# Kernel optimization log

Hardware: AMD Instinct MI355X
Metric: run time of the kernel (lower is better)

Reference implementation:

```python
import jax, jax.numpy as jnp
import numpy as np

D_MODEL = 2048
N_HEADS = 32
N_KV = 8
N_REP = N_HEADS // N_KV  # 4
HEAD_DIM = D_MODEL // N_HEADS  # 64
ROPE_BASE = 10000.0
B, T = 2, 2048


def rope_tables(seq_len, head_dim):
    inv_freq = 1.0 / (ROPE_BASE ** (jnp.arange(0, head_dim, 2, dtype=jnp.float32) / head_dim))
    t = jnp.arange(seq_len, dtype=jnp.float32)
    freqs = jnp.outer(t, inv_freq)            # [T, hd/2]
    emb = jnp.concatenate([freqs, freqs], -1)  # [T, hd]
    return jnp.cos(emb), jnp.sin(emb)


def rotate_half(x):
    x1, x2 = jnp.split(x, 2, axis=-1)
    return jnp.concatenate([-x2, x1], axis=-1)


def setup_inputs() -> dict:
    key = jax.random.key(0)
    ks = jax.random.split(key, 5)
    s = D_MODEL ** -0.5
    return {
        "x": jax.random.normal(ks[0], (B, T, D_MODEL), jnp.float32),
        "Wq": jax.random.normal(ks[1], (D_MODEL, D_MODEL), jnp.float32) * s,
        "Wk": jax.random.normal(ks[2], (D_MODEL, N_KV * HEAD_DIM), jnp.float32) * s,
        "Wv": jax.random.normal(ks[3], (D_MODEL, N_KV * HEAD_DIM), jnp.float32) * s,
        "Wo": jax.random.normal(ks[4], (D_MODEL, D_MODEL), jnp.float32) * s,
    }


def reference(x, Wq, Wk, Wv, Wo):
    Bx, Tx, C = x.shape
    # QKV projections -> [B, H, T, hd]
    q = (x @ Wq).reshape(Bx, Tx, N_HEADS, HEAD_DIM).transpose(0, 2, 1, 3)
    k = (x @ Wk).reshape(Bx, Tx, N_KV, HEAD_DIM).transpose(0, 2, 1, 3)
    v = (x @ Wv).reshape(Bx, Tx, N_KV, HEAD_DIM).transpose(0, 2, 1, 3)
    # RoPE (offset=0, no cache -> prefill path)
    cos, sin = rope_tables(Tx, HEAD_DIM)  # [T, hd]
    cos = cos[None, None]
    sin = sin[None, None]
    q = q * cos + rotate_half(q) * sin
    k = k * cos + rotate_half(k) * sin
    # Grouped causal attention without materializing expanded KV:
    # q grouped as [B, n_kv, n_rep, T, hd] shares each kv head across n_rep q heads.
    scale = HEAD_DIM ** -0.5
    qg = q.reshape(Bx, N_KV, N_REP, Tx, HEAD_DIM)
    scores = jnp.einsum('bgrtd,bgsd->bgrts', qg, k) * scale  # [B, g, r, T, S]
    causal = jnp.tril(jnp.ones((Tx, Tx), dtype=bool))
    scores = jnp.where(causal, scores, jnp.float32(-jnp.inf))
    attn = jax.nn.softmax(scores, axis=-1)
    out = jnp.einsum('bgrts,bgsd->bgrtd', attn, v)  # [B, g, r, T, hd]
    out = out.reshape(Bx, N_HEADS, Tx, HEAD_DIM).transpose(0, 2, 1, 3).reshape(Bx, Tx, C)
    return out @ Wo, k, v
```

## Files before the change

kernel.cpp:

```cpp
#include <hip/hip_runtime.h>
#include <hip/hip_bf16.h>
#include <cstdint>

typedef uint16_t u16;
typedef __attribute__((ext_vector_type(8))) __bf16 bf16x8;
typedef __attribute__((ext_vector_type(4))) float f32x4;
typedef __attribute__((ext_vector_type(16))) float f32x16;
typedef __attribute__((ext_vector_type(8))) unsigned short u16x8;

#define GLD_LDS(SRC, DST) \
  __builtin_amdgcn_global_load_lds((const __attribute__((address_space(1))) void*)(SRC), \
                                   (__attribute__((address_space(3))) void*)(DST), 16, 0, 0)

__device__ __forceinline__ u16 f2bf(float f) {
  uint32_t u = __float_as_uint(f);
  u += 0x7fffu + ((u >> 16) & 1u);
  return (u16)(u >> 16);
}

__device__ __forceinline__ uint32_t pk2(float a, float b) {
  union { __bf16 h[2]; uint32_t u; } x;
  x.h[0] = (__bf16)a; x.h[1] = (__bf16)b;
  return x.u;
}

__device__ __forceinline__ float fexp2(float x) {
#if __has_builtin(__builtin_amdgcn_exp2f)
  return __builtin_amdgcn_exp2f(x);
#else
  return exp2f(x);
#endif
}

__global__ void cast_f32_bf16(const float* __restrict__ in, u16* __restrict__ out, int n4) {
  int i = blockIdx.x * blockDim.x + threadIdx.x;
  if (i < n4) {
    const float4 v = reinterpret_cast<const float4*>(in)[i];
    ushort4 o;
    o.x = f2bf(v.x); o.y = f2bf(v.y); o.z = f2bf(v.z); o.w = f2bf(v.w);
    reinterpret_cast<ushort4*>(out)[i] = o;
  }
}

__global__ void transpose_cast(const float* __restrict__ W, u16* __restrict__ Wt, int K, int N) {
  __shared__ float tile[32][33];
  int n0 = blockIdx.x * 32, k0 = blockIdx.y * 32;
  int tx = threadIdx.x, ty = threadIdx.y;
  #pragma unroll
  for (int i = ty; i < 32; i += 8)
    tile[i][tx] = W[(size_t)(k0 + i) * N + n0 + tx];
  __syncthreads();
  #pragma unroll
  for (int i = ty; i < 32; i += 8)
    Wt[(size_t)(n0 + i) * K + k0 + tx] = f2bf(tile[tx][i]);
}

__global__ void rope_tables_k(float* __restrict__ cosT, float* __restrict__ sinT) {
  int t = blockIdx.x, i = threadIdx.x;
  float invf = powf(10000.0f, -(float)i * (1.0f / 32.0f));
  float ang = (float)t * invf;
  cosT[t * 32 + i] = cosf(ang);
  sinT[t * 32 + i] = sinf(ang);
}

__global__ __launch_bounds__(512, 2) void gemm256(const u16* __restrict__ A,
    const u16* __restrict__ Bt, float* __restrict__ C, int M, int N, int K) {
  __shared__ alignas(16) u16 Asm[2][2][256][32];
  __shared__ alignas(16) u16 Bsm[2][2][256][32];

  const int tid = threadIdx.x;
  const int l = tid & 63;
  const int w = tid >> 6;
  const int wm = w >> 2, wn = w & 3;
  const int l15 = l & 15, l4 = l >> 4;
  const int m0 = blockIdx.y * 256, n0 = blockIdx.x * 256;
  const int NT = K >> 6;

  f32x4 acc[8][4] = {};

  const int srow = tid >> 2;
  const int sg   = (tid & 3) ^ ((srow >> 1) & 3);
  const u16* Ag = A + (size_t)(m0 + srow) * K + sg * 8;
  const u16* Bg = Bt + (size_t)(n0 + srow) * K + sg * 8;
  const size_t rsk = (size_t)128 * K;
  char* AsD = (char*)&Asm[0][0][0][0] + tid * 16;
  char* BsD = (char*)&Bsm[0][0][0][0] + tid * 16;

#define STAGE_A(BUF, KH, KT) do { \
    GLD_LDS(Ag + (KT) + (KH) * 32,       AsD + ((BUF) * 2 + (KH)) * 16384); \
    GLD_LDS(Ag + (KT) + (KH) * 32 + rsk, AsD + ((BUF) * 2 + (KH)) * 16384 + 8192); \
  } while (0)
#define STAGE_B(BUF, KH, KT) do { \
    GLD_LDS(Bg + (KT) + (KH) * 32,       BsD + ((BUF) * 2 + (KH)) * 16384); \
    GLD_LDS(Bg + (KT) + (KH) * 32 + rsk, BsD + ((BUF) * 2 + (KH)) * 16384 + 8192); \
  } while (0)

  STAGE_A(0, 0, 0);  STAGE_B(0, 0, 0);
  STAGE_A(0, 1, 0);  STAGE_B(0, 1, 0);
  STAGE_A(1, 0, 64); STAGE_B(1, 0, 64);

  const int swz = (l15 >> 1) & 3;

  for (int t = 0; t < NT; ++t) {
    const int c = t & 1;
    const int ktn  = (t + 1) << 6;
    const int ktn2 = (t + 2) << 6;
    bf16x8 bfv[4], af[4];

    if (t < NT - 1) { asm volatile("s_waitcnt vmcnt(8)" ::: "memory"); }
    else            { asm volatile("s_waitcnt vmcnt(4)" ::: "memory"); }
    asm volatile("s_barrier" ::: "memory");
    #pragma unroll
    for (int mf = 0; mf < 4; ++mf)
      af[mf] = *(const bf16x8*)&Asm[c][0][wm * 128 + mf * 16 + l15][(l4 ^ swz) * 8];
    #pragma unroll
    for (int nf = 0; nf < 4; ++nf)
      bfv[nf] = *(const bf16x8*)&Bsm[c][0][wn * 64 + nf * 16 + l15][(l4 ^ swz) * 8];
    if (t + 1 < NT) STAGE_A(c ^ 1, 1, ktn);
    __builtin_amdgcn_s_setprio(1);
    #pragma unroll
    for (int mf = 0; mf < 4; ++mf)
      #pragma unroll
      for (int nf = 0; nf < 4; ++nf)
        acc[mf][nf] = __builtin_amdgcn_mfma_f32_16x16x32_bf16(af[mf], bfv[nf], acc[mf][nf], 0, 0, 0);
    __builtin_amdgcn_s_setprio(0);
    asm volatile("s_barrier" ::: "memory");

    #pragma unroll
    for (int mf = 0; mf < 4; ++mf)
      af[mf] = *(const bf16x8*)&Asm[c][0][wm * 128 + 64 + mf * 16 + l15][(l4 ^ swz) * 8];
    if (t + 1 < NT) STAGE_B(c ^ 1, 1, ktn);
    __builtin_amdgcn_s_setprio(1);
    #pragma unroll
    for (int mf = 0; mf < 4; ++mf)
      #pragma unroll
      for (int nf = 0; nf < 4; ++nf)
        acc[4 + mf][nf] = __builtin_amdgcn_mfma_f32_16x16x32_bf16(af[mf], bfv[nf], acc[4 + mf][nf], 0, 0, 0);
    __builtin_amdgcn_s_setprio(0);
    asm volatile("s_barrier" ::: "memory");

    if (t < NT - 1) { asm volatile("s_waitcnt vmcnt(8)" ::: "memory"); }
    else            { asm volatile("s_waitcnt vmcnt(0)" ::: "memory"); }
    asm volatile("s_barrier" ::: "memory");
    #pragma unroll
    for (int mf = 0; mf < 4; ++mf)
      af[mf] = *(const bf16x8*)&Asm[c][1][wm * 128 + mf * 16 + l15][(l4 ^ swz) * 8];
    #pragma unroll
    for (int nf = 0; nf < 4; ++nf)
      bfv[nf] = *(const bf16x8*)&Bsm[c][1][wn * 64 + nf * 16 + l15][(l4 ^ swz) * 8];
    if (t + 2 < NT) STAGE_A(c, 0, ktn2);
    __builtin_amdgcn_s_setprio(1);
    #pragma unroll
    for (int mf = 0; mf < 4; ++mf)
      #pragma unroll
      for (int nf = 0; nf < 4; ++nf)
        acc[mf][nf] = __builtin_amdgcn_mfma_f32_16x16x32_bf16(af[mf], bfv[nf], acc[mf][nf], 0, 0, 0);
    __builtin_amdgcn_s_setprio(0);
    asm volatile("s_barrier" ::: "memory");

    #pragma unroll
    for (int mf = 0; mf < 4; ++mf)
      af[mf] = *(const bf16x8*)&Asm[c][1][wm * 128 + 64 + mf * 16 + l15][(l4 ^ swz) * 8];
    if (t + 2 < NT) STAGE_B(c, 0, ktn2);
    __builtin_amdgcn_s_setprio(1);
    #pragma unroll
    for (int mf = 0; mf < 4; ++mf)
      #pragma unroll
      for (int nf = 0; nf < 4; ++nf)
        acc[4 + mf][nf] = __builtin_amdgcn_mfma_f32_16x16x32_bf16(af[mf], bfv[nf], acc[4 + mf][nf], 0, 0, 0);
    __builtin_amdgcn_s_setprio(0);
    asm volatile("s_barrier" ::: "memory");
  }
#undef STAGE_A
#undef STAGE_B

  #pragma unroll
  for (int mi = 0; mi < 8; ++mi)
    #pragma unroll
    for (int nf = 0; nf < 4; ++nf)
      #pragma unroll
      for (int r = 0; r < 4; ++r) {
        int row = m0 + wm * 128 + mi * 16 + l4 * 4 + r;
        int col = n0 + wn * 64 + nf * 16 + l15;
        C[(size_t)row * N + col] = acc[mi][nf][r];
      }
}

__global__ __launch_bounds__(256) void rope_scatter(const float* __restrict__ QKV,
    const float* __restrict__ cosT, const float* __restrict__ sinT,
    u16* __restrict__ Qr, u16* __restrict__ Kr,
    float* __restrict__ outK, float* __restrict__ outV) {
  const float QSCALE = 0.125f * 1.44269504088896f;
  int row = blockIdx.x;
  int b = row >> 11, t = row & 2047;
  const float* src = QKV + (size_t)row * 3072;
  int tid = threadIdx.x;
  #pragma unroll
  for (int p = tid; p < 1024; p += 256) {
    int h = p >> 5, d = p & 31;
    float c = cosT[t * 32 + d], s = sinT[t * 32 + d];
    float q0 = src[h * 64 + d], q1 = src[h * 64 + d + 32];
    size_t base = ((size_t)(b * 32 + h) * 2048 + t) * 64 + d;
    Qr[base]      = f2bf((q0 * c - q1 * s) * QSCALE);
    Qr[base + 32] = f2bf((q1 * c + q0 * s) * QSCALE);
  }
  {
    int p = tid;
    int gk = p >> 5, d = p & 31;
    float c = cosT[t * 32 + d], s = sinT[t * 32 + d];
    float k0 = src[2048 + gk * 64 + d], k1 = src[2048 + gk * 64 + d + 32];
    float r0 = k0 * c - k1 * s, r1 = k1 * c + k0 * s;
    size_t base = ((size_t)(b * 8 + gk) * 2048 + t) * 64 + d;
    Kr[base] = f2bf(r0); Kr[base + 32] = f2bf(r1);
    outK[base] = r0; outK[base + 32] = r1;
  }
  #pragma unroll
  for (int p = tid; p < 512; p += 256) {
    int gv = p >> 6, d = p & 63;
    size_t base = ((size_t)(b * 8 + gv) * 2048 + t) * 64 + d;
    outV[base] = src[2560 + gv * 64 + d];
  }
}

__global__ __launch_bounds__(256) void v_transpose(const float* __restrict__ src, u16* __restrict__ dst) {
  __shared__ float tile[64][65];
  int tt = blockIdx.x, bg = blockIdx.y;
  int tid = threadIdx.x;
  const float* sp = src + (size_t)bg * 2048 * 64 + (size_t)tt * 64 * 64;
  int tl = tid >> 2, c0 = (tid & 3) * 16;
  #pragma unroll
  for (int i = 0; i < 4; ++i) {
    float4 v = *reinterpret_cast<const float4*>(sp + (size_t)tl * 64 + c0 + i * 4);
    tile[tl][c0 + i * 4 + 0] = v.x;
    tile[tl][c0 + i * 4 + 1] = v.y;
    tile[tl][c0 + i * 4 + 2] = v.z;
    tile[tl][c0 + i * 4 + 3] = v.w;
  }
  __syncthreads();
  int d = tid >> 2, j0 = (tid & 3) * 16;
  u16x8 a, c;
  #pragma unroll
  for (int j = 0; j < 8; ++j) a[j] = f2bf(tile[j0 + j][d]);
  #pragma unroll
  for (int j = 0; j < 8; ++j) c[j] = f2bf(tile[j0 + 8 + j][d]);
  u16* dp = dst + (size_t)bg * 64 * 2048 + (size_t)d * 2048 + tt * 64 + j0;
  *reinterpret_cast<u16x8*>(dp) = a;
  *reinterpret_cast<u16x8*>(dp + 8) = c;
}

__global__ __launch_bounds__(256) void attn_kernel(
    const u16* __restrict__ Qr, const u16* __restrict__ Kr,
    const u16* __restrict__ Vt, u16* __restrict__ Ao) {
  __shared__ alignas(16) u16 Ks[2][64][72];
  __shared__ alignas(16) u16 Vs[2][64][72];

  const float FIXEDM = 24.0f;

  int bid = blockIdx.x;
  int pairI = bid >> 5;
  int sub = (bid >> 4) & 1;
  int g   = (bid >> 1) & 7;
  int b   = bid & 1;
  int tid = threadIdx.x;
  int w = tid >> 6, l = tid & 63;
  int l31 = l & 31, hi = l >> 5;
  int h = g * 4 + w;

  const u16* Kh = Kr + (size_t)(b * 8 + g) * 2048 * 64;
  const u16* Vh = Vt + (size_t)(b * 8 + g) * 64 * 2048;

  union { u16x8 u; bf16x8 v; } ones;
  #pragma unroll
  for (int i = 0; i < 8; ++i) ones.u[i] = 0x3F80;

  int srow = tid >> 2, sc0 = (tid & 3) * 16;
  const u16* Kp = Kh + (size_t)srow * 64 + sc0;
  const u16* Vp = Vh + (size_t)srow * 2048 + sc0;

  for (int half = 0; half < 2; ++half) {
    const int qc  = half ? pairI : (31 - pairI);
    const int q0w = qc * 64 + sub * 32;
    const int qg  = q0w + l31;

    const u16* Qh = Qr + ((size_t)(b * 32 + h) * 2048 + q0w) * 64;
    bf16x8 qf[4];
    #pragma unroll
    for (int t = 0; t < 4; ++t)
      qf[t] = *reinterpret_cast<const bf16x8*>(Qh + (size_t)l31 * 64 + t * 16 + hi * 8);

    f32x16 o0 = {}, o1 = {}, lacc = {};

    if (half) __syncthreads();

    {
      bf16x8 k0v = *reinterpret_cast<const bf16x8*>(Kp);
      bf16x8 k1v = *reinterpret_cast<const bf16x8*>(Kp + 8);
      bf16x8 v0v = *reinterpret_cast<const bf16x8*>(Vp);
      bf16x8 v1v = *reinterpret_cast<const bf16x8*>(Vp + 8);
      *reinterpret_cast<bf16x8*>(&Ks[0][srow][sc0]) = k0v;
      *reinterpret_cast<bf16x8*>(&Ks[0][srow][sc0 + 8]) = k1v;
      *reinterpret_cast<bf16x8*>(&Vs[0][srow][sc0]) = v0v;
      *reinterpret_cast<bf16x8*>(&Vs[0][srow][sc0 + 8]) = v1v;
    }
    __syncthreads();

    for (int s = 0; s <= qc; ++s) {
      int cur = s & 1;
      bf16x8 knx0, knx1, vnx0, vnx1;
      if (s < qc) {
        knx0 = *reinterpret_cast<const bf16x8*>(Kp + (size_t)(s + 1) * 4096);
        knx1 = *reinterpret_cast<const bf16x8*>(Kp + (size_t)(s + 1) * 4096 + 8);
        vnx0 = *reinterpret_cast<const bf16x8*>(Vp + (size_t)(s + 1) * 64);
        vnx1 = *reinterpret_cast<const bf16x8*>(Vp + (size_t)(s + 1) * 64 + 8);
      }
      int nh = (s == qc && sub == 0) ? 1 : 2;

      f32x16 s0 = {}, s1 = {};
      __builtin_amdgcn_s_setprio(1);
      #pragma unroll
      for (int t = 0; t < 4; ++t) {
        bf16x8 kf0 = *reinterpret_cast<const bf16x8*>(&Ks[cur][l31][t * 16 + hi * 8]);
        s0 = __builtin_amdgcn_mfma_f32_32x32x16_bf16(kf0, qf[t], s0, 0, 0, 0);
      }
      if (nh == 2) {
        #pragma unroll
        for (int t = 0; t < 4; ++t) {
          bf16x8 kf1 = *reinterpret_cast<const bf16x8*>(&Ks[cur][32 + l31][t * 16 + hi * 8]);
          s1 = __builtin_amdgcn_mfma_f32_32x32x16_bf16(kf1, qf[t], s1, 0, 0, 0);
        }
      }
      __builtin_amdgcn_s_setprio(0);

      if (s == qc) {
        #pragma unroll
        for (int r = 0; r < 16; ++r) {
          int kvg = s * 64 + (r & 3) + (r >> 2) * 8 + hi * 4;
          if (kvg > qg) s0[r] = -INFINITY;
        }
        if (nh == 2) {
          #pragma unroll
          for (int r = 0; r < 16; ++r) {
            int kvg = s * 64 + 32 + (r & 3) + (r >> 2) * 8 + hi * 4;
            if (kvg > qg) s1[r] = -INFINITY;
          }
        }
      }

      float p0[16], p1[16];
      #pragma unroll
      for (int r = 0; r < 16; ++r) p0[r] = fexp2(s0[r] - FIXEDM);
      if (nh == 2) {
        #pragma unroll
        for (int r = 0; r < 16; ++r) p1[r] = fexp2(s1[r] - FIXEDM);
      }

      uint32_t pkA[8], pkB[8];
      #pragma unroll
      for (int gi = 0; gi < 8; ++gi) {
        if (gi < nh * 4) {
          const float* pp = (gi < 4) ? p0 : p1;
          int base = (gi & 3) * 4;
          pkA[gi] = pk2(pp[base + 0], pp[base + 1]);
          pkB[gi] = pk2(pp[base + 2], pp[base + 3]);
        }
      }
      __builtin_amdgcn_s_setprio(1);
      #pragma unroll
      for (int kc = 0; kc < 4; ++kc) {
        if (kc < nh * 2) {
          uint32_t zA = pkA[kc * 2 + (hi ^ 1)];
          uint32_t zB = pkB[kc * 2 + (hi ^ 1)];
          uint32_t sA = (uint32_t)__shfl_xor((int)zA, 32);
          uint32_t sB = (uint32_t)__shfl_xor((int)zB, 32);
          uint32_t oA = pkA[kc * 2 + hi];
          uint32_t oB = pkB[kc * 2 + hi];
          union { uint32_t wd[4]; bf16x8 v; } pb;
          pb.wd[0] = hi ? sA : oA;
          pb.wd[1] = hi ? sB : oB;
          pb.wd[2] = hi ? oA : sA;
          pb.wd[3] = hi ? oB : sB;
          bf16x8 va0 = *reinterpret_cast<const bf16x8*>(&Vs[cur][l31][kc * 16 + hi * 8]);
          bf16x8 va1 = *reinterpret_cast<const bf16x8*>(&Vs[cur][32 + l31][kc * 16 + hi * 8]);
          o0 = __builtin_amdgcn_mfma_f32_32x32x16_bf16(va0, pb.v, o0, 0, 0, 0);
          o1 = __builtin_amdgcn_mfma_f32_32x32x16_bf16(va1, pb.v, o1, 0, 0, 0);
          lacc = __builtin_amdgcn_mfma_f32_32x32x16_bf16(ones.v, pb.v, lacc, 0, 0, 0);
        }
      }
      __builtin_amdgcn_s_setprio(0);

      if (s < qc) {
        *reinterpret_cast<bf16x8*>(&Ks[cur ^ 1][srow][sc0]) = knx0;
        *reinterpret_cast<bf16x8*>(&Ks[cur ^ 1][srow][sc0 + 8]) = knx1;
        *reinterpret_cast<bf16x8*>(&Vs[cur ^ 1][srow][sc0]) = vnx0;
        *reinterpret_cast<bf16x8*>(&Vs[cur ^ 1][srow][sc0 + 8]) = vnx1;
        __syncthreads();
      }
    }

    float inv = 1.0f / lacc[0];
    int token = b * 2048 + q0w + l31;
    u16* dst = Ao + (size_t)token * 2048 + h * 64;
    #pragma unroll
    for (int hf = 0; hf < 2; ++hf) {
      f32x16 ov = hf ? o1 : o0;
      #pragma unroll
      for (int r = 0; r < 16; r += 2) {
        int d = (r & 3) + (r >> 2) * 8 + hi * 4 + hf * 32;
        *reinterpret_cast<uint32_t*>(dst + d) = pk2(ov[r] * inv, ov[r + 1] * inv);
      }
    }
  }
}

extern "C" void kernel_launch(void* const* d_in, const int* in_sizes, int n_in,
                              void* d_out, int out_size, void* d_ws, size_t ws_size,
                              hipStream_t stream) {
  const float* x  = (const float*)d_in[0];
  const float* Wq = (const float*)d_in[1];
  const float* Wk = (const float*)d_in[2];
  const float* Wv = (const float*)d_in[3];
  const float* Wo = (const float*)d_in[4];
  float* out = (float*)d_out;

  char* ws = (char*)d_ws;
  u16*   Xb    = (u16*)(ws + 0);
  u16*   Wcat  = (u16*)(ws + 16777216);
  u16*   WoT   = (u16*)(ws + 29360128);
  float* QKV   = (float*)(ws + 37748736);
  u16*   AttnB = (u16*)(ws + 37748736);
  u16*   Qr    = (u16*)(ws + 88080384);
  u16*   Kr    = (u16*)(ws + 104857600);
  u16*   Vtr   = (u16*)(ws + 109051904);
  float* cosT  = (float*)(ws + 113246208);
  float* sinT  = (float*)(ws + 113508352);

  float* outK = out + 8388608;
  float* outV = out + 10485760;

  cast_f32_bf16<<<8192, 256, 0, stream>>>(x, Xb, 2097152);
  transpose_cast<<<dim3(64, 64), dim3(32, 8), 0, stream>>>(Wq, Wcat, 2048, 2048);
  transpose_cast<<<dim3(16, 64), dim3(32, 8), 0, stream>>>(Wk, Wcat + 2048 * 2048, 2048, 512);
  transpose_cast<<<dim3(16, 64), dim3(32, 8), 0, stream>>>(Wv, Wcat + 2560 * 2048, 2048, 512);
  transpose_cast<<<dim3(64, 64), dim3(32, 8), 0, stream>>>(Wo, WoT, 2048, 2048);
  rope_tables_k<<<2048, 32, 0, stream>>>(cosT, sinT);
  gemm256<<<dim3(12, 16), 512, 0, stream>>>(Xb, Wcat, QKV, 4096, 3072, 2048);
  rope_scatter<<<4096, 256, 0, stream>>>(QKV, cosT, sinT, Qr, Kr, outK, outV);
  v_transpose<<<dim3(32, 16), 256, 0, stream>>>(outV, Vtr);
  attn_kernel<<<512, 256, 0, stream>>>(Qr, Kr, Vtr, AttnB);
  gemm256<<<dim3(8, 16), 512, 0, stream>>>(AttnB, WoT, out, 4096, 2048, 2048);
}
```

Baseline: 238.2 us.

## Load K/V MFMA fragments directly from global memory instead of LDS staging

Removes the double-buffered LDS tiles for K and V and the per-iteration __syncthreads. Each wave now reads its MFMA operand fragments straight from global memory (relying on L1/L2 since the four waves share the same KV head). It also raises launch bounds to request 4 blocks per CU. This trades LDS traffic and barriers for redundant global loads with no software prefetch, so load latency is exposed inside the MFMA loop.

```diff
diff --git a/kernel.cpp b/kernel.cpp
--- a/kernel.cpp
+++ b/kernel.cpp
@@ -248,12 +248,9 @@
   *reinterpret_cast<u16x8*>(dp + 8) = c;
 }
 
-__global__ __launch_bounds__(256) void attn_kernel(
+__global__ __launch_bounds__(256, 4) void attn_kernel(
     const u16* __restrict__ Qr, const u16* __restrict__ Kr,
     const u16* __restrict__ Vt, u16* __restrict__ Ao) {
-  __shared__ alignas(16) u16 Ks[2][64][72];
-  __shared__ alignas(16) u16 Vs[2][64][72];
-
   const float FIXEDM = 24.0f;
 
   int bid = blockIdx.x;
@@ -269,13 +266,12 @@
   const u16* Kh = Kr + (size_t)(b * 8 + g) * 2048 * 64;
   const u16* Vh = Vt + (size_t)(b * 8 + g) * 64 * 2048;
 
+  const u16* Kl = Kh + (size_t)l31 * 64 + hi * 8;
+  const u16* Vl = Vh + (size_t)l31 * 2048 + hi * 8;
+
   union { u16x8 u; bf16x8 v; } ones;
   #pragma unroll
   for (int i = 0; i < 8; ++i) ones.u[i] = 0x3F80;
-
-  int srow = tid >> 2, sc0 = (tid & 3) * 16;
-  const u16* Kp = Kh + (size_t)srow * 64 + sc0;
-  const u16* Vp = Vh + (size_t)srow * 2048 + sc0;
 
   for (int half = 0; half < 2; ++half) {
     const int qc  = half ? pairI : (31 - pairI);
@@ -290,42 +286,22 @@
 
     f32x16 o0 = {}, o1 = {}, lacc = {};
 
-    if (half) __syncthreads();
-
-    {
-      bf16x8 k0v = *reinterpret_cast<const bf16x8*>(Kp);
-      bf16x8 k1v = *reinterpret_cast<const bf16x8*>(Kp + 8);
-      bf16x8 v0v = *reinterpret_cast<const bf16x8*>(Vp);
-      bf16x8 v1v = *reinterpret_cast<const bf16x8*>(Vp + 8);
-      *reinterpret_cast<bf16x8*>(&Ks[0][srow][sc0]) = k0v;
-      *reinterpret_cast<bf16x8*>(&Ks[0][srow][sc0 + 8]) = k1v;
-      *reinterpret_cast<bf16x8*>(&Vs[0][srow][sc0]) = v0v;
-      *reinterpret_cast<bf16x8*>(&Vs[0][srow][sc0 + 8]) = v1v;
-    }
-    __syncthreads();
-
     for (int s = 0; s <= qc; ++s) {
-      int cur = s & 1;
-      bf16x8 knx0, knx1, vnx0, vnx1;
-      if (s < qc) {
-        knx0 = *reinterpret_cast<const bf16x8*>(Kp + (size_t)(s + 1) * 4096);
-        knx1 = *reinterpret_cast<const bf16x8*>(Kp + (size_t)(s + 1) * 4096 + 8);
-        vnx0 = *reinterpret_cast<const bf16x8*>(Vp + (size_t)(s + 1) * 64);
-        vnx1 = *reinterpret_cast<const bf16x8*>(Vp + (size_t)(s + 1) * 64 + 8);
-      }
+      const u16* Ksp = Kl + (size_t)s * 4096;
+      const u16* Vsp = Vl + s * 64;
       int nh = (s == qc && sub == 0) ? 1 : 2;
 
       f32x16 s0 = {}, s1 = {};
       __builtin_amdgcn_s_setprio(1);
       #pragma unroll
       for (int t = 0; t < 4; ++t) {
-        bf16x8 kf0 = *reinterpret_cast<const bf16x8*>(&Ks[cur][l31][t * 16 + hi * 8]);
+        bf16x8 kf0 = *reinterpret_cast<const bf16x8*>(Ksp + t * 16);
         s0 = __builtin_amdgcn_mfma_f32_32x32x16_bf16(kf0, qf[t], s0, 0, 0, 0);
       }
       if (nh == 2) {
         #pragma unroll
         for (int t = 0; t < 4; ++t) {
-          bf16x8 kf1 = *reinterpret_cast<const bf16x8*>(&Ks[cur][32 + l31][t * 16 + hi * 8]);
+          bf16x8 kf1 = *reinterpret_cast<const bf16x8*>(Ksp + 2048 + t * 16);
           s1 = __builtin_amdgcn_mfma_f32_32x32x16_bf16(kf1, qf[t], s1, 0, 0, 0);
         }
       }
@@ -379,22 +355,14 @@
           pb.wd[1] = hi ? sB : oB;
           pb.wd[2] = hi ? oA : sA;
           pb.wd[3] = hi ? oB : sB;
-          bf16x8 va0 = *reinterpret_cast<const bf16x8*>(&Vs[cur][l31][kc * 16 + hi * 8]);
-          bf16x8 va1 = *reinterpret_cast<const bf16x8*>(&Vs[cur][32 + l31][kc * 16 + hi * 8]);
+          bf16x8 va0 = *reinterpret_cast<const bf16x8*>(Vsp + kc * 16);
+          bf16x8 va1 = *reinterpret_cast<const bf16x8*>(Vsp + 65536 + kc * 16);
           o0 = __builtin_amdgcn_mfma_f32_32x32x16_bf16(va0, pb.v, o0, 0, 0, 0);
           o1 = __builtin_amdgcn_mfma_f32_32x32x16_bf16(va1, pb.v, o1, 0, 0, 0);
           lacc = __builtin_amdgcn_mfma_f32_32x32x16_bf16(ones.v, pb.v, lacc, 0, 0, 0);
         }
       }
       __builtin_amdgcn_s_setprio(0);
-
-      if (s < qc) {
-        *reinterpret_cast<bf16x8*>(&Ks[cur ^ 1][srow][sc0]) = knx0;
-        *reinterpret_cast<bf16x8*>(&Ks[cur ^ 1][srow][sc0 + 8]) = knx1;
-        *reinterpret_cast<bf16x8*>(&Vs[cur ^ 1][srow][sc0]) = vnx0;
-        *reinterpret_cast<bf16x8*>(&Vs[cur ^ 1][srow][sc0 + 8]) = vnx1;
-        __syncthreads();
-      }
     }
 
     float inv = 1.0f / lacc[0];
```

Measured after the change: 388.1 us. 1.63x slower.

## Emit bf16 QKV from projection GEMM and merge attention sub-blocks into 512-thread blocks

Applied to the files above, without the earlier changes.

The QKV projection GEMM now writes bf16 instead of fp32, which halves the intermediate write and the read in rope_scatter. The returned K and V outputs are then rebuilt from bf16-rounded values, so they lose precision. Separately, the attention kernel merges the two 32-row query sub-blocks into one 512-thread block. Each K/V tile is then loaded to shared memory once for both halves, with each thread loading half as much, and the block count is halved.

```diff
diff --git a/kernel.cpp b/kernel.cpp
--- a/kernel.cpp
+++ b/kernel.cpp
@@ -16,6 +16,10 @@
   uint32_t u = __float_as_uint(f);
   u += 0x7fffu + ((u >> 16) & 1u);
   return (u16)(u >> 16);
+}
+
+__device__ __forceinline__ float bf2f(u16 u) {
+  return __uint_as_float(((uint32_t)u) << 16);
 }
 
 __device__ __forceinline__ uint32_t pk2(float a, float b) {
@@ -63,8 +67,9 @@
   sinT[t * 32 + i] = sinf(ang);
 }
 
+template<bool BF16OUT>
 __global__ __launch_bounds__(512, 2) void gemm256(const u16* __restrict__ A,
-    const u16* __restrict__ Bt, float* __restrict__ C, int M, int N, int K) {
+    const u16* __restrict__ Bt, void* __restrict__ Cv, int M, int N, int K) {
   __shared__ alignas(16) u16 Asm[2][2][256][32];
   __shared__ alignas(16) u16 Bsm[2][2][256][32];
 
@@ -182,24 +187,25 @@
       for (int r = 0; r < 4; ++r) {
         int row = m0 + wm * 128 + mi * 16 + l4 * 4 + r;
         int col = n0 + wn * 64 + nf * 16 + l15;
-        C[(size_t)row * N + col] = acc[mi][nf][r];
-      }
-}
-
-__global__ __launch_bounds__(256) void rope_scatter(const float* __restrict__ QKV,
+        if (BF16OUT) ((u16*)Cv)[(size_t)row * N + col] = f2bf(acc[mi][nf][r]);
+        else         ((float*)Cv)[(size_t)row * N + col] = acc[mi][nf][r];
+      }
+}
+
+__global__ __launch_bounds__(256) void rope_scatter(const u16* __restrict__ QKV,
     const float* __restrict__ cosT, const float* __restrict__ sinT,
     u16* __restrict__ Qr, u16* __restrict__ Kr,
     float* __restrict__ outK, float* __restrict__ outV) {
   const float QSCALE = 0.125f * 1.44269504088896f;
   int row = blockIdx.x;
   int b = row >> 11, t = row & 2047;
-  const float* src = QKV + (size_t)row * 3072;
+  const u16* src = QKV + (size_t)row * 3072;
   int tid = threadIdx.x;
   #pragma unroll
   for (int p = tid; p < 1024; p += 256) {
     int h = p >> 5, d = p & 31;
     float c = cosT[t * 32 + d], s = sinT[t * 32 + d];
-    float q0 = src[h * 64 + d], q1 = src[h * 64 + d + 32];
+    float q0 = bf2f(src[h * 64 + d]), q1 = bf2f(src[h * 64 + d + 32]);
     size_t base = ((size_t)(b * 32 + h) * 2048 + t) * 64 + d;
     Qr[base]      = f2bf((q0 * c - q1 * s) * QSCALE);
     Qr[base + 32] = f2bf((q1 * c + q0 * s) * QSCALE);
@@ -208,7 +214,7 @@
     int p = tid;
     int gk = p >> 5, d = p & 31;
     float c = cosT[t * 32 + d], s = sinT[t * 32 + d];
-    float k0 = src[2048 + gk * 64 + d], k1 = src[2048 + gk * 64 + d + 32];
+    float k0 = bf2f(src[2048 + gk * 64 + d]), k1 = bf2f(src[2048 + gk * 64 + d + 32]);
     float r0 = k0 * c - k1 * s, r1 = k1 * c + k0 * s;
     size_t base = ((size_t)(b * 8 + gk) * 2048 + t) * 64 + d;
     Kr[base] = f2bf(r0); Kr[base + 32] = f2bf(r1);
@@ -218,7 +224,7 @@
   for (int p = tid; p < 512; p += 256) {
     int gv = p >> 6, d = p & 63;
     size_t base = ((size_t)(b * 8 + gv) * 2048 + t) * 64 + d;
-    outV[base] = src[2560 + gv * 64 + d];
+    outV[base] = bf2f(src[2560 + gv * 64 + d]);
   }
 }
 
@@ -248,7 +254,7 @@
   *reinterpret_cast<u16x8*>(dp + 8) = c;
 }
 
-__global__ __launch_bounds__(256) void attn_kernel(
+__global__ __launch_bounds__(512) void attn_kernel(
     const u16* __restrict__ Qr, const u16* __restrict__ Kr,
     const u16* __restrict__ Vt, u16* __restrict__ Ao) {
   __shared__ alignas(16) u16 Ks[2][64][72];
@@ -257,14 +263,14 @@
   const float FIXEDM = 24.0f;
 
   int bid = blockIdx.x;
-  int pairI = bid >> 5;
-  int sub = (bid >> 4) & 1;
+  int pairI = bid >> 4;
   int g   = (bid >> 1) & 7;
   int b   = bid & 1;
   int tid = threadIdx.x;
   int w = tid >> 6, l = tid & 63;
   int l31 = l & 31, hi = l >> 5;
-  int h = g * 4 + w;
+  int h = g * 4 + (w & 3);
+  int sub = w >> 2;
 
   const u16* Kh = Kr + (size_t)(b * 8 + g) * 2048 * 64;
   const u16* Vh = Vt + (size_t)(b * 8 + g) * 64 * 2048;
@@ -273,7 +279,7 @@
   #pragma unroll
   for (int i = 0; i < 8; ++i) ones.u[i] = 0x3F80;
 
-  int srow = tid >> 2, sc0 = (tid & 3) * 16;
+  int srow = tid >> 3, sc0 = (tid & 7) * 8;
   const u16* Kp = Kh + (size_t)srow * 64 + sc0;
   const u16* Vp = Vh + (size_t)srow * 2048 + sc0;
 
@@ -294,24 +300,18 @@
 
     {
       bf16x8 k0v = *reinterpret_cast<const bf16x8*>(Kp);
-      bf16x8 k1v = *reinterpret_cast<const bf16x8*>(Kp + 8);
       bf16x8 v0v = *reinterpret_cast<const bf16x8*>(Vp);
-      bf16x8 v1v = *reinterpret_cast<const bf16x8*>(Vp + 8);
       *reinterpret_cast<bf16x8*>(&Ks[0][srow][sc0]) = k0v;
-      *reinterpret_cast<bf16x8*>(&Ks[0][srow][sc0 + 8]) = k1v;
       *reinterpret_cast<bf16x8*>(&Vs[0][srow][sc0]) = v0v;
-      *reinterpret_cast<bf16x8*>(&Vs[0][srow][sc0 + 8]) = v1v;
     }
     __syncthreads();
 
     for (int s = 0; s <= qc; ++s) {
       int cur = s & 1;
-      bf16x8 knx0, knx1, vnx0, vnx1;
+      bf16x8 knx, vnx;
       if (s < qc) {
-        knx0 = *reinterpret_cast<const bf16x8*>(Kp + (size_t)(s + 1) * 4096);
-        knx1 = *reinterpret_cast<const bf16x8*>(Kp + (size_t)(s + 1) * 4096 + 8);
-        vnx0 = *reinterpret_cast<const bf16x8*>(Vp + (size_t)(s + 1) * 64);
-        vnx1 = *reinterpret_cast<const bf16x8*>(Vp + (size_t)(s + 1) * 64 + 8);
+        knx = *reinterpret_cast<const bf16x8*>(Kp + (size_t)(s + 1) * 4096);
+        vnx = *reinterpret_cast<const bf16x8*>(Vp + (size_t)(s + 1) * 64);
       }
       int nh = (s == qc && sub == 0) ? 1 : 2;
 
@@ -389,10 +389,8 @@
       __builtin_amdgcn_s_setprio(0);
 
       if (s < qc) {
-        *reinterpret_cast<bf16x8*>(&Ks[cur ^ 1][srow][sc0]) = knx0;
-        *reinterpret_cast<bf16x8*>(&Ks[cur ^ 1][srow][sc0 + 8]) = knx1;
-        *reinterpret_cast<bf16x8*>(&Vs[cur ^ 1][srow][sc0]) = vnx0;
-        *reinterpret_cast<bf16x8*>(&Vs[cur ^ 1][srow][sc0 + 8]) = vnx1;
+        *reinterpret_cast<bf16x8*>(&Ks[cur ^ 1][srow][sc0]) = knx;
+        *reinterpret_cast<bf16x8*>(&Vs[cur ^ 1][srow][sc0]) = vnx;
         __syncthreads();
       }
     }
@@ -426,7 +424,7 @@
   u16*   Xb    = (u16*)(ws + 0);
   u16*   Wcat  = (u16*)(ws + 16777216);
   u16*   WoT   = (u16*)(ws + 29360128);
-  float* QKV   = (float*)(ws + 37748736);
+  u16*   QKV   = (u16*)(ws + 37748736);
   u16*   AttnB = (u16*)(ws + 37748736);
   u16*   Qr    = (u16*)(ws + 88080384);
   u16*   Kr    = (u16*)(ws + 104857600);
@@ -443,9 +441,9 @@
   transpose_cast<<<dim3(16, 64), dim3(32, 8), 0, stream>>>(Wv, Wcat + 2560 * 2048, 2048, 512);
   transpose_cast<<<dim3(64, 64), dim3(32, 8), 0, stream>>>(Wo, WoT, 2048, 2048);
   rope_tables_k<<<2048, 32, 0, stream>>>(cosT, sinT);
-  gemm256<<<dim3(12, 16), 512, 0, stream>>>(Xb, Wcat, QKV, 4096, 3072, 2048);
+  gemm256<true><<<dim3(12, 16), 512, 0, stream>>>(Xb, Wcat, QKV, 4096, 3072, 2048);
   rope_scatter<<<4096, 256, 0, stream>>>(QKV, cosT, sinT, Qr, Kr, outK, outV);
   v_transpose<<<dim3(32, 16), 256, 0, stream>>>(outV, Vtr);
-  attn_kernel<<<512, 256, 0, stream>>>(Qr, Kr, Vtr, AttnB);
-  gemm256<<<dim3(8, 16), 512, 0, stream>>>(AttnB, WoT, out, 4096, 2048, 2048);
-}
+  attn_kernel<<<256, 512, 0, stream>>>(Qr, Kr, Vtr, AttnB);
+  gemm256<false><<<dim3(8, 16), 512, 0, stream>>>(AttnB, WoT, out, 4096, 2048, 2048);
+}
```

Result: no change. 241.2 us (+1.3%).
